# Optimization experiments

Measured on AMD Instinct MI355X. Metric: run time of the kernel, lower is better.

## Reference

```python
import jax, jax.numpy as jnp
import numpy as np


def segment_softmax(scores, seg, num_segments):
    # numerically stable softmax over edges grouped by destination node
    m = jax.ops.segment_max(scores, seg, num_segments=num_segments)
    e = jnp.exp(scores - m[seg])
    d = jax.ops.segment_sum(e, seg, num_segments=num_segments)
    return e / d[seg]


def setup_inputs() -> dict:
    key = jax.random.key(0)
    ks = jax.random.split(key, 13)
    N, E, D = 50000, 400000, 128
    s = 0.02
    return {
        "x": jax.random.normal(ks[0], (N, D), dtype=jnp.float32),
        "t": jax.random.normal(ks[1], (N, D), dtype=jnp.float32),
        "edge_index": jax.random.randint(ks[2], (2, E), 0, N),
        "W_x": jax.random.normal(ks[3], (D, D), dtype=jnp.float32) * s,
        "W_t": jax.random.normal(ks[4], (D, D), dtype=jnp.float32) * s,
        "Q_alpha_w": jax.random.normal(ks[5], (D, D), dtype=jnp.float32) * s,
        "Q_alpha_b": jax.random.normal(ks[6], (D,), dtype=jnp.float32) * s,
        "K_alpha_w": jax.random.normal(ks[7], (D, D), dtype=jnp.float32) * s,
        "K_alpha_b": jax.random.normal(ks[8], (D,), dtype=jnp.float32) * s,
        "Q_beta_w": jax.random.normal(ks[9], (D, D), dtype=jnp.float32) * s,
        "Q_beta_b": jax.random.normal(ks[10], (D,), dtype=jnp.float32) * s,
        "K_beta_w": jax.random.normal(ks[11], (D, D), dtype=jnp.float32) * s,
        "K_beta_b": jax.random.normal(ks[12], (D,), dtype=jnp.float32) * s,
    }


def reference(x, t, edge_index, W_x, W_t, Q_alpha_w, Q_alpha_b,
              K_alpha_w, K_alpha_b, Q_beta_w, Q_beta_b, K_beta_w, K_beta_b):
    N, D = x.shape
    row, col = edge_index[0], edge_index[1]  # row = dest (i), col = src (j)
    inv_sqrt_d = 1.0 / (D ** 0.5)

    # Linear projections on nodes, then gather per edge (same math as
    # projecting the gathered edge features, since Linear is per-row).
    q_alpha = (t @ Q_alpha_w.T + Q_alpha_b)[row]   # [E, D]
    k_alpha = (t @ K_alpha_w.T + K_alpha_b)[col]   # [E, D]
    alpha_scores = jnp.sum(q_alpha * k_alpha, axis=-1) * inv_sqrt_d  # [E]
    alpha = segment_softmax(alpha_scores, row, N)  # [E]

    q_beta = (x @ Q_beta_w.T + Q_beta_b)[row]
    k_beta = (x @ K_beta_w.T + K_beta_b)[col]
    beta_scores = jnp.sum(q_beta * k_beta, axis=-1) * inv_sqrt_d
    beta = segment_softmax(beta_scores, row, N)

    msg_for_t = alpha[:, None] * (t @ W_t.T)[col]  # [E, D]
    msg_for_x = beta[:, None] * (x @ W_x.T)[col]   # [E, D]

    out_x = jax.ops.segment_sum(msg_for_x, row, num_segments=N)  # [N, D]
    out_t = jax.ops.segment_sum(msg_for_t, row, num_segments=N)  # [N, D]
    return (out_x, out_t)
```

## Files before the change

kernel.cpp:

```cpp
#include <hip/hip_runtime.h>

__device__ __forceinline__ unsigned short f2bf(float f) {
    unsigned int x = __float_as_uint(f);
    x += 0x7fffu + ((x >> 16) & 1u);
    return (unsigned short)(x >> 16);
}
__device__ __forceinline__ float2 bf2x(unsigned int u) {
    float2 r;
    r.x = __uint_as_float(u << 16);
    r.y = __uint_as_float(u & 0xffff0000u);
    return r;
}
__device__ __forceinline__ float bcastf(float v, int l) {
    return __uint_as_float(__builtin_amdgcn_readlane(__float_as_uint(v), l));
}
template <int PAT>
__device__ __forceinline__ float swzadd(float v) {
    return v + __uint_as_float(__builtin_amdgcn_ds_swizzle(__float_as_uint(v), PAT));
}

typedef __attribute__((ext_vector_type(8))) short frag8;
typedef __attribute__((ext_vector_type(4))) float fragf4;

__global__ __launch_bounds__(256) void convert_hist(
    const float* __restrict__ s0, const float* __restrict__ s1,
    const float* __restrict__ s2, const float* __restrict__ s3,
    const float* __restrict__ s4, const float* __restrict__ s5,
    unsigned short* __restrict__ dst,
    const int* __restrict__ row, int* __restrict__ deg, int E)
{
    const int b = blockIdx.x;
    if (b < 96) {
        int id = b * 256 + threadIdx.x;
        int m = id >> 12;
        int e = (id & 4095) * 4;
        const float* s = (m == 0) ? s0 : (m == 1) ? s1 : (m == 2) ? s2
                       : (m == 3) ? s3 : (m == 4) ? s4 : s5;
        float4 v = *(const float4*)(s + e);
        int r = e >> 7, c = e & 127;
        int ct = r >> 4, li = r & 15;
        int ks = c >> 5, quad = (c >> 3) & 3, j = c & 7;
        ushort4 u;
        u.x = f2bf(v.x); u.y = f2bf(v.y); u.z = f2bf(v.z); u.w = f2bf(v.w);
        *(ushort4*)(dst + m * 16384 +
                    ((size_t)((ct * 4 + ks) * 64 + quad * 16 + li)) * 8 + j) = u;
    } else {
        int e = (b - 96) * 256 + threadIdx.x;
        if (e < E) atomicAdd(&deg[row[e]], 1);
    }
}

#define TLROW 72
__global__ __launch_bounds__(256, 4) void proj_scatter(
    const float* __restrict__ in_t, const float* __restrict__ in_x, int N,
    const unsigned short* __restrict__ Wbf,
    const float* __restrict__ Qa_b, const float* __restrict__ Ka_b,
    const float* __restrict__ Qb_b, const float* __restrict__ Kb_b,
    unsigned short* __restrict__ qa, unsigned short* __restrict__ qb,
    unsigned short* __restrict__ kab, unsigned short* __restrict__ twxw,
    const int* __restrict__ erow, const int* __restrict__ ecol,
    int* __restrict__ cursor, int* __restrict__ csr_col, int E,
    int nScat, int nbx)
{
    __shared__ __align__(16) unsigned short tile[4][2][16 * TLROW];

    if ((int)blockIdx.x < nScat) {
        int e = blockIdx.x * 256 + threadIdx.x;
        if (e < E) {
            int p = atomicAdd(&cursor[erow[e]], 1);
            csr_col[p] = ecol[e];
        }
        return;
    }
    const int pb = blockIdx.x - nScat;
    const int bx = pb % nbx;
    const int rest = pb / nbx;
    const int p = rest & 1;
    const int cth = rest >> 1;

    const int wave = threadIdx.x >> 6;
    const int lane = threadIdx.x & 63;
    const int li = lane & 15, quad = lane >> 4;
    const int r0 = (bx * 4 + wave) * 16;
    if (r0 >= N) return;
    const int r = r0 + li;
    const bool rv = r < N;

    frag8 bt[4];
    {
        const float* inp = p ? in_x : in_t;
        const float* st = inp + (size_t)r * 128 + quad * 8;
#pragma unroll
        for (int ks = 0; ks < 4; ks++) {
            float4 lo = make_float4(0.f, 0.f, 0.f, 0.f), hi = lo;
            if (rv) {
                lo = *(const float4*)(st + ks * 32);
                hi = *(const float4*)(st + ks * 32 + 4);
            }
            frag8 f;
            f[0] = (short)f2bf(lo.x); f[1] = (short)f2bf(lo.y);
            f[2] = (short)f2bf(lo.z); f[3] = (short)f2bf(lo.w);
            f[4] = (short)f2bf(hi.x); f[5] = (short)f2bf(hi.y);
            f[6] = (short)f2bf(hi.z); f[7] = (short)f2bf(hi.w);
            bt[ks] = f;
        }
    }

    int buf = 0;
    auto phase = [&](int m, const float* bias,
                     unsigned short* dst, int rstride, int coff) {
        const unsigned short* wb = Wbf + (size_t)m * 16384 + (size_t)cth * 8192
                                 + (size_t)lane * 8;
        frag8 af[16];
#pragma unroll
        for (int u = 0; u < 16; u++)
            af[u] = *(const frag8*)(wb + u * 512);

        fragf4 acc[4];
#pragma unroll
        for (int ct = 0; ct < 4; ct++) acc[ct] = (fragf4){0.f, 0.f, 0.f, 0.f};
#pragma unroll
        for (int ct = 0; ct < 4; ct++) {
#pragma unroll
            for (int ks = 0; ks < 4; ks++)
                acc[ct] = __builtin_amdgcn_mfma_f32_16x16x32_bf16(
                    af[ct * 4 + ks], bt[ks], acc[ct], 0, 0, 0);
        }

        unsigned short* lt = &tile[wave][buf][0];
#pragma unroll
        for (int ct = 0; ct < 4; ct++) {
            const int c = ct * 16 + quad * 4;
            float4 bv = make_float4(0.f, 0.f, 0.f, 0.f);
            if (bias) bv = *(const float4*)(bias + cth * 64 + c);
            ushort4 u;
            u.x = f2bf(acc[ct][0] + bv.x);
            u.y = f2bf(acc[ct][1] + bv.y);
            u.z = f2bf(acc[ct][2] + bv.z);
            u.w = f2bf(acc[ct][3] + bv.w);
            *(ushort4*)&lt[li * TLROW + c] = u;
        }
#pragma unroll
        for (int it = 0; it < 2; it++) {
            const int rr = it * 8 + (lane >> 3);
            const int cg = lane & 7;
            if (r0 + rr < N) {
                uint4 v = *(const uint4*)&lt[rr * TLROW + cg * 8];
                *(uint4*)(dst + (size_t)(r0 + rr) * rstride + coff + cg * 8) = v;
            }
        }
        buf ^= 1;
    };

    const int ch = cth * 64;
    if (p == 0) {
        phase(0, Qa_b, qa,   128, ch);
        phase(1, Ka_b, kab,  256, ch);
        phase(2, nullptr, twxw, 256, ch);
    } else {
        phase(3, Qb_b, qb,   128, ch);
        phase(4, Kb_b, kab,  256, 128 + ch);
        phase(5, nullptr, twxw, 256, 128 + ch);
    }
}

#define SCAN_CHUNK 2048

__device__ __forceinline__ int wave_incl_scan(int v, int lane) {
#pragma unroll
    for (int d = 1; d < 64; d <<= 1) {
        int u = __shfl_up(v, d, 64);
        if (lane >= d) v += u;
    }
    return v;
}

__global__ __launch_bounds__(256) void scan_partial(const int* __restrict__ deg,
                                                    int* __restrict__ partial, int N) {
    const int tid = threadIdx.x;
    const int base = blockIdx.x * SCAN_CHUNK + tid * 8;
    int s = 0;
#pragma unroll
    for (int j = 0; j < 8; j++) {
        int i = base + j;
        s += (i < N) ? deg[i] : 0;
    }
    const int lane = tid & 63;
    s = wave_incl_scan(s, lane);
    __shared__ int wsum[4];
    if (lane == 63) wsum[tid >> 6] = s;
    __syncthreads();
    if (tid == 0) partial[blockIdx.x] = wsum[0] + wsum[1] + wsum[2] + wsum[3];
}

__global__ __launch_bounds__(64) void scan_base(int* __restrict__ partial, int nb,
                                                int* __restrict__ offs, int N) {
    const int lane = threadIdx.x;
    int v = (lane < nb) ? partial[lane] : 0;
    int inc = wave_incl_scan(v, lane);
    if (lane < nb) partial[lane] = inc - v;
    if (lane == 63) offs[N] = inc;
}

__global__ __launch_bounds__(256) void scan_final(const int* __restrict__ deg,
                                                  const int* __restrict__ partial,
                                                  int* __restrict__ offs,
                                                  int* __restrict__ cursor, int N) {
    const int tid = threadIdx.x;
    const int lane = tid & 63;
    const int wv = tid >> 6;
    const int base = blockIdx.x * SCAN_CHUNK + tid * 8;
    int v[8];
    int s = 0;
#pragma unroll
    for (int j = 0; j < 8; j++) {
        int i = base + j;
        v[j] = (i < N) ? deg[i] : 0;
        s += v[j];
    }
    int incl = wave_incl_scan(s, lane);
    __shared__ int wsum[4];
    if (lane == 63) wsum[wv] = incl;
    __syncthreads();
    int wbase = 0;
#pragma unroll
    for (int w = 0; w < 4; w++) wbase += (w < wv) ? wsum[w] : 0;
    int run = partial[blockIdx.x] + wbase + incl - s;
#pragma unroll
    for (int j = 0; j < 8; j++) {
        int i = base + j;
        if (i < N) { offs[i] = run; cursor[i] = run; }
        run += v[j];
    }
}

__global__ __launch_bounds__(256) void edge_fused(
    const unsigned short* __restrict__ qa, const unsigned short* __restrict__ qb,
    const unsigned short* __restrict__ kab, const unsigned short* __restrict__ twxw,
    const int* __restrict__ csr_col, const int* __restrict__ offs,
    float* __restrict__ out_x, float* __restrict__ out_t, int N)
{
    const int n = blockIdx.x * 4 + (threadIdx.x >> 6);
    if (n >= N) return;
    const int lane = threadIdx.x & 63;
    const int g = lane >> 4, sub = lane & 15;
    const int s = offs[n], end = offs[n + 1];

    float qaf[8], qbf[8];
    {
        uint4 a = *(const uint4*)(qa + (size_t)n * 128 + sub * 8);
        uint4 b = *(const uint4*)(qb + (size_t)n * 128 + sub * 8);
        float2 f;
        f = bf2x(a.x); qaf[0] = f.x; qaf[1] = f.y;
        f = bf2x(a.y); qaf[2] = f.x; qaf[3] = f.y;
        f = bf2x(a.z); qaf[4] = f.x; qaf[5] = f.y;
        f = bf2x(a.w); qaf[6] = f.x; qaf[7] = f.y;
        f = bf2x(b.x); qbf[0] = f.x; qbf[1] = f.y;
        f = bf2x(b.y); qbf[2] = f.x; qbf[3] = f.y;
        f = bf2x(b.z); qbf[4] = f.x; qbf[5] = f.y;
        f = bf2x(b.w); qbf[6] = f.x; qbf[7] = f.y;
    }

    const float scale = 0.08838834764831845f;
    const bool xside = lane >= 32;
    const unsigned short* vbase = twxw + lane * 4;
    float acc0 = 0.f, acc1 = 0.f, acc2 = 0.f, acc3 = 0.f, dd = 0.f;

    if (end > s) {
        int c = csr_col[min(s + g, end - 1)];
        for (int i0 = s; i0 < end; i0 += 4) {
            const bool val = (i0 + g) < end;
            const int idx = i0 + 4 + g;
            const int cn = csr_col[(idx < end) ? idx : (end - 1)];

            const int c0 = __builtin_amdgcn_readlane(c, 0);
            const int c1 = __builtin_amdgcn_readlane(c, 16);
            const int c2 = __builtin_amdgcn_readlane(c, 32);
            const int c3 = __builtin_amdgcn_readlane(c, 48);
            const uint2 gv0 = *(const uint2*)(vbase + (size_t)c0 * 256);
            const uint2 gv1 = *(const uint2*)(vbase + (size_t)c1 * 256);
            const uint2 gv2 = *(const uint2*)(vbase + (size_t)c2 * 256);
            const uint2 gv3 = *(const uint2*)(vbase + (size_t)c3 * 256);

            const unsigned short* kp = kab + (size_t)c * 256 + sub * 8;
            const uint4 ka4 = *(const uint4*)kp;
            const uint4 kb4 = *(const uint4*)(kp + 128);
            float pa = 0.f, pb = 0.f;
            {
                float2 f;
                f = bf2x(ka4.x); pa = fmaf(qaf[0], f.x, fmaf(qaf[1], f.y, pa));
                f = bf2x(ka4.y); pa = fmaf(qaf[2], f.x, fmaf(qaf[3], f.y, pa));
                f = bf2x(ka4.z); pa = fmaf(qaf[4], f.x, fmaf(qaf[5], f.y, pa));
                f = bf2x(ka4.w); pa = fmaf(qaf[6], f.x, fmaf(qaf[7], f.y, pa));
                f = bf2x(kb4.x); pb = fmaf(qbf[0], f.x, fmaf(qbf[1], f.y, pb));
                f = bf2x(kb4.y); pb = fmaf(qbf[2], f.x, fmaf(qbf[3], f.y, pb));
                f = bf2x(kb4.z); pb = fmaf(qbf[4], f.x, fmaf(qbf[5], f.y, pb));
                f = bf2x(kb4.w); pb = fmaf(qbf[6], f.x, fmaf(qbf[7], f.y, pb));
            }
            pa = swzadd<0x041F>(pa); pb = swzadd<0x041F>(pb);
            pa = swzadd<0x081F>(pa); pb = swzadd<0x081F>(pb);
            pa = swzadd<0x101F>(pa); pb = swzadd<0x101F>(pb);
            pa = swzadd<0x201F>(pa); pb = swzadd<0x201F>(pb);

            const float ea = val ? __expf(fminf(pa * scale, 60.f)) : 0.f;
            const float eb = val ? __expf(fminf(pb * scale, 60.f)) : 0.f;

            const float w0 = xside ? bcastf(eb, 0)  : bcastf(ea, 0);
            const float w1 = xside ? bcastf(eb, 16) : bcastf(ea, 16);
            const float w2 = xside ? bcastf(eb, 32) : bcastf(ea, 32);
            const float w3 = xside ? bcastf(eb, 48) : bcastf(ea, 48);

            float2 lo, hi;
            lo = bf2x(gv0.x); hi = bf2x(gv0.y);
            dd += w0;
            acc0 = fmaf(w0, lo.x, acc0); acc1 = fmaf(w0, lo.y, acc1);
            acc2 = fmaf(w0, hi.x, acc2); acc3 = fmaf(w0, hi.y, acc3);
            lo = bf2x(gv1.x); hi = bf2x(gv1.y);
            dd += w1;
            acc0 = fmaf(w1, lo.x, acc0); acc1 = fmaf(w1, lo.y, acc1);
            acc2 = fmaf(w1, hi.x, acc2); acc3 = fmaf(w1, hi.y, acc3);
            lo = bf2x(gv2.x); hi = bf2x(gv2.y);
            dd += w2;
            acc0 = fmaf(w2, lo.x, acc0); acc1 = fmaf(w2, lo.y, acc1);
            acc2 = fmaf(w2, hi.x, acc2); acc3 = fmaf(w2, hi.y, acc3);
            lo = bf2x(gv3.x); hi = bf2x(gv3.y);
            dd += w3;
            acc0 = fmaf(w3, lo.x, acc0); acc1 = fmaf(w3, lo.y, acc1);
            acc2 = fmaf(w3, hi.x, acc2); acc3 = fmaf(w3, hi.y, acc3);

            c = cn;
        }
    }

    const float r = (dd > 0.f) ? 1.f / dd : 0.f;
    float4 o = make_float4(acc0 * r, acc1 * r, acc2 * r, acc3 * r);
    float* op = xside ? (out_x + (size_t)n * 128 + (lane - 32) * 4)
                      : (out_t + (size_t)n * 128 + lane * 4);
    *(float4*)op = o;
}

extern "C" void kernel_launch(void* const* d_in, const int* in_sizes, int n_in,
                              void* d_out, int out_size, void* d_ws, size_t ws_size,
                              hipStream_t stream) {
    const float* x    = (const float*)d_in[0];
    const float* t    = (const float*)d_in[1];
    const int*   ei   = (const int*)d_in[2];
    const float* W_x  = (const float*)d_in[3];
    const float* W_t  = (const float*)d_in[4];
    const float* Qa_w = (const float*)d_in[5];
    const float* Qa_b = (const float*)d_in[6];
    const float* Ka_w = (const float*)d_in[7];
    const float* Ka_b = (const float*)d_in[8];
    const float* Qb_w = (const float*)d_in[9];
    const float* Qb_b = (const float*)d_in[10];
    const float* Kb_w = (const float*)d_in[11];
    const float* Kb_b = (const float*)d_in[12];

    const int N = in_sizes[0] / 128;
    const int E = in_sizes[2] / 2;
    const int* row = ei;
    const int* col = ei + E;

    char* ws = (char*)d_ws;
    size_t off = 0;
    auto carve = [&](size_t bytes) -> void* {
        void* p = ws + off;
        off += (bytes + 255) & ~(size_t)255;
        return p;
    };
    unsigned short* qa   = (unsigned short*)carve((size_t)N * 128 * 2);
    unsigned short* qb   = (unsigned short*)carve((size_t)N * 128 * 2);
    unsigned short* kab  = (unsigned short*)carve((size_t)N * 256 * 2);
    unsigned short* twxw = (unsigned short*)carve((size_t)N * 256 * 2);
    int* deg      = (int*)carve((size_t)N * 4);
    int* cursor   = (int*)carve((size_t)N * 4);
    int* offs     = (int*)carve((size_t)(N + 1) * 4);
    int* csr_col  = (int*)carve((size_t)E * 4);
    const int nscan = (N + SCAN_CHUNK - 1) / SCAN_CHUNK;
    int* partial  = (int*)carve((size_t)nscan * 4);
    unsigned short* Wbf = (unsigned short*)carve((size_t)6 * 16384 * 2);

    (void)hipMemsetAsync(deg, 0, (size_t)N * 4, stream);

    dim3 b256(256);
    const int nHist = (E + 255) / 256;
    convert_hist<<<dim3(96 + nHist), b256, 0, stream>>>(
        Qa_w, Ka_w, W_t, Qb_w, Kb_w, W_x, Wbf, row, deg, E);

    scan_partial<<<dim3(nscan), b256, 0, stream>>>(deg, partial, N);
    scan_base<<<dim3(1), dim3(64), 0, stream>>>(partial, nscan, offs, N);
    scan_final<<<dim3(nscan), b256, 0, stream>>>(deg, partial, offs, cursor, N);

    const int nbx = (N + 63) / 64;
    const int nScat = (E + 255) / 256;
    proj_scatter<<<dim3(nScat + nbx * 4), b256, 0, stream>>>(
        t, x, N, Wbf, Qa_b, Ka_b, Qb_b, Kb_b, qa, qb, kab, twxw,
        row, col, cursor, csr_col, E, nScat, nbx);

    float* out_x = (float*)d_out;
    float* out_t = out_x + (size_t)N * 128;
    edge_fused<<<dim3((N + 3) / 4), b256, 0, stream>>>(
        qa, qb, kab, twxw, csr_col, offs, out_x, out_t, N);
}
```

Baseline: 262.7 us.

## Fold key projection into query weights and apply value projection after aggregation

Precomputes Wq^T·Wk (scaled) and Wk^T·bq so the score becomes (q')·t_j on raw bf16 node features, removing the per-node key projections. The key bias is dropped because it is constant within each softmax segment. The edge kernel now gathers only raw t/x rows (512 B per edge instead of separate key and value gathers) and aggregates with one node per 16-lane group. The W_t/W_x projection is then applied per 16-node tile with MFMA after aggregation, by linearity. This cuts projection work and gather traffic, at the cost of extra bf16 rounding of raw features and aggregates, and less parallelism per node in the edge loop.

```diff
diff --git a/kernel.cpp b/kernel.cpp
--- a/kernel.cpp
+++ b/kernel.cpp
@@ -11,9 +11,6 @@
     r.y = __uint_as_float(u & 0xffff0000u);
     return r;
 }
-__device__ __forceinline__ float bcastf(float v, int l) {
-    return __uint_as_float(__builtin_amdgcn_readlane(__float_as_uint(v), l));
-}
 template <int PAT>
 __device__ __forceinline__ float swzadd(float v) {
     return v + __uint_as_float(__builtin_amdgcn_ds_swizzle(__float_as_uint(v), PAT));
@@ -22,30 +19,86 @@
 typedef __attribute__((ext_vector_type(8))) short frag8;
 typedef __attribute__((ext_vector_type(4))) float fragf4;
 
-__global__ __launch_bounds__(256) void convert_hist(
-    const float* __restrict__ s0, const float* __restrict__ s1,
-    const float* __restrict__ s2, const float* __restrict__ s3,
-    const float* __restrict__ s4, const float* __restrict__ s5,
-    unsigned short* __restrict__ dst,
+
+__global__ __launch_bounds__(256) void prep_convert_hist(
+    const float* __restrict__ Qa_w, const float* __restrict__ Ka_w,
+    const float* __restrict__ Qa_b,
+    const float* __restrict__ Qb_w, const float* __restrict__ Kb_w,
+    const float* __restrict__ Qb_b,
+    const float* __restrict__ W_t, const float* __restrict__ W_x,
+    unsigned short* __restrict__ Wbf, float* __restrict__ ba, float* __restrict__ bb,
     const int* __restrict__ row, int* __restrict__ deg, int E)
 {
     const int b = blockIdx.x;
-    if (b < 96) {
-        int id = b * 256 + threadIdx.x;
-        int m = id >> 12;
-        int e = (id & 4095) * 4;
-        const float* s = (m == 0) ? s0 : (m == 1) ? s1 : (m == 2) ? s2
-                       : (m == 3) ? s3 : (m == 4) ? s4 : s5;
-        float4 v = *(const float4*)(s + e);
-        int r = e >> 7, c = e & 127;
+    const int tid = threadIdx.x;
+    const float sc = 0.08838834764831845f;
+
+    if (b < 2) {
+        const int m = b;
+        const float* Kw = m ? Kb_w : Ka_w;
+        const float* Qw = m ? Qb_w : Qa_w;
+        const float* bq = m ? Qb_b : Qa_b;
+        const int r0l = (tid & 31) * 4;
+        const int c0l = (tid >> 5) * 16;
+        float a0[16], a1[16], a2[16], a3[16];
+#pragma unroll
+        for (int j = 0; j < 16; j++) { a0[j] = 0.f; a1[j] = 0.f; a2[j] = 0.f; a3[j] = 0.f; }
+#pragma unroll 2
+        for (int ch = 0; ch < 128; ch++) {
+            const float* kr = Kw + ch * 128;
+            const float* qr = Qw + ch * 128;
+            float4 kv = *(const float4*)(kr + r0l);
+            float4 q0 = *(const float4*)(qr + c0l);
+            float4 q1 = *(const float4*)(qr + c0l + 4);
+            float4 q2v = *(const float4*)(qr + c0l + 8);
+            float4 q3 = *(const float4*)(qr + c0l + 12);
+            float qv[16] = {q0.x,q0.y,q0.z,q0.w, q1.x,q1.y,q1.z,q1.w,
+                            q2v.x,q2v.y,q2v.z,q2v.w, q3.x,q3.y,q3.z,q3.w};
+#pragma unroll
+            for (int j = 0; j < 16; j++) {
+                a0[j] = fmaf(kv.x, qv[j], a0[j]);
+                a1[j] = fmaf(kv.y, qv[j], a1[j]);
+                a2[j] = fmaf(kv.z, qv[j], a2[j]);
+                a3[j] = fmaf(kv.w, qv[j], a3[j]);
+            }
+        }
+        unsigned short* base = Wbf + (size_t)m * 16384;
+#pragma unroll
+        for (int i = 0; i < 4; i++) {
+            const float* ai = (i == 0) ? a0 : (i == 1) ? a1 : (i == 2) ? a2 : a3;
+            const int r = r0l + i, ct = r >> 4, li = r & 15;
+#pragma unroll
+            for (int jb = 0; jb < 2; jb++) {
+                const int c = c0l + jb * 8;
+                const int ks = c >> 5, quad = (c >> 3) & 3;
+                frag8 u;
+#pragma unroll
+                for (int j = 0; j < 8; j++) u[j] = (short)f2bf(ai[jb * 8 + j] * sc);
+                *(frag8*)(base + ((size_t)((ct * 4 + ks) * 64 + quad * 16 + li)) * 8) = u;
+            }
+        }
+        if (tid < 128) {
+            float a = 0.f;
+#pragma unroll 8
+            for (int ch = 0; ch < 128; ch++) a = fmaf(bq[ch], Kw[ch * 128 + tid], a);
+            (m ? bb : ba)[tid] = a * sc;
+        }
+    } else if (b < 34) {
+        const int cm = (b - 2) >> 4;
+        const int local = (b - 2) & 15;
+        const int id = local * 256 + tid;
+        const int e4 = id * 4;
+        const float* s = cm ? W_x : W_t;
+        float4 v = *(const float4*)(s + e4);
+        int r = e4 >> 7, c = e4 & 127;
         int ct = r >> 4, li = r & 15;
         int ks = c >> 5, quad = (c >> 3) & 3, j = c & 7;
         ushort4 u;
         u.x = f2bf(v.x); u.y = f2bf(v.y); u.z = f2bf(v.z); u.w = f2bf(v.w);
-        *(ushort4*)(dst + m * 16384 +
+        *(ushort4*)(Wbf + (size_t)(2 + cm) * 16384 +
                     ((size_t)((ct * 4 + ks) * 64 + quad * 16 + li)) * 8 + j) = u;
     } else {
-        int e = (b - 96) * 256 + threadIdx.x;
+        int e = (b - 34) * 256 + tid;
         if (e < E) atomicAdd(&deg[row[e]], 1);
     }
 }
@@ -54,15 +107,13 @@
 __global__ __launch_bounds__(256, 4) void proj_scatter(
     const float* __restrict__ in_t, const float* __restrict__ in_x, int N,
     const unsigned short* __restrict__ Wbf,
-    const float* __restrict__ Qa_b, const float* __restrict__ Ka_b,
-    const float* __restrict__ Qb_b, const float* __restrict__ Kb_b,
-    unsigned short* __restrict__ qa, unsigned short* __restrict__ qb,
-    unsigned short* __restrict__ kab, unsigned short* __restrict__ twxw,
+    const float* __restrict__ ba, const float* __restrict__ bb,
+    unsigned short* __restrict__ q2ab, unsigned short* __restrict__ txb,
     const int* __restrict__ erow, const int* __restrict__ ecol,
     int* __restrict__ cursor, int* __restrict__ csr_col, int E,
     int nScat, int nbx)
 {
-    __shared__ __align__(16) unsigned short tile[4][2][16 * TLROW];
+    __shared__ __align__(16) unsigned short tile[4][16 * TLROW];
 
     if ((int)blockIdx.x < nScat) {
         int e = blockIdx.x * 256 + threadIdx.x;
@@ -106,61 +157,52 @@
         }
     }
 
-    int buf = 0;
-    auto phase = [&](int m, const float* bias,
-                     unsigned short* dst, int rstride, int coff) {
-        const unsigned short* wb = Wbf + (size_t)m * 16384 + (size_t)cth * 8192
-                                 + (size_t)lane * 8;
-        frag8 af[16];
-#pragma unroll
-        for (int u = 0; u < 16; u++)
-            af[u] = *(const frag8*)(wb + u * 512);
-
-        fragf4 acc[4];
-#pragma unroll
-        for (int ct = 0; ct < 4; ct++) acc[ct] = (fragf4){0.f, 0.f, 0.f, 0.f};
-#pragma unroll
-        for (int ct = 0; ct < 4; ct++) {
-#pragma unroll
-            for (int ks = 0; ks < 4; ks++)
-                acc[ct] = __builtin_amdgcn_mfma_f32_16x16x32_bf16(
-                    af[ct * 4 + ks], bt[ks], acc[ct], 0, 0, 0);
-        }
-
-        unsigned short* lt = &tile[wave][buf][0];
-#pragma unroll
-        for (int ct = 0; ct < 4; ct++) {
-            const int c = ct * 16 + quad * 4;
-            float4 bv = make_float4(0.f, 0.f, 0.f, 0.f);
-            if (bias) bv = *(const float4*)(bias + cth * 64 + c);
-            ushort4 u;
-            u.x = f2bf(acc[ct][0] + bv.x);
-            u.y = f2bf(acc[ct][1] + bv.y);
-            u.z = f2bf(acc[ct][2] + bv.z);
-            u.w = f2bf(acc[ct][3] + bv.w);
-            *(ushort4*)&lt[li * TLROW + c] = u;
-        }
-#pragma unroll
-        for (int it = 0; it < 2; it++) {
-            const int rr = it * 8 + (lane >> 3);
-            const int cg = lane & 7;
-            if (r0 + rr < N) {
-                uint4 v = *(const uint4*)&lt[rr * TLROW + cg * 8];
-                *(uint4*)(dst + (size_t)(r0 + rr) * rstride + coff + cg * 8) = v;
-            }
-        }
-        buf ^= 1;
-    };
-
-    const int ch = cth * 64;
-    if (p == 0) {
-        phase(0, Qa_b, qa,   128, ch);
-        phase(1, Ka_b, kab,  256, ch);
-        phase(2, nullptr, twxw, 256, ch);
-    } else {
-        phase(3, Qb_b, qb,   128, ch);
-        phase(4, Kb_b, kab,  256, 128 + ch);
-        phase(5, nullptr, twxw, 256, 128 + ch);
+    if (cth == 0 && rv) {
+#pragma unroll
+        for (int ks = 0; ks < 4; ks++)
+            *(frag8*)(txb + (size_t)r * 256 + p * 128 + ks * 32 + quad * 8) = bt[ks];
+    }
+
+    const unsigned short* wb = Wbf + (size_t)p * 16384 + (size_t)cth * 8192
+                             + (size_t)lane * 8;
+    frag8 af[16];
+#pragma unroll
+    for (int u = 0; u < 16; u++)
+        af[u] = *(const frag8*)(wb + u * 512);
+
+    fragf4 acc[4];
+#pragma unroll
+    for (int ct = 0; ct < 4; ct++) acc[ct] = (fragf4){0.f, 0.f, 0.f, 0.f};
+#pragma unroll
+    for (int ct = 0; ct < 4; ct++) {
+#pragma unroll
+        for (int ks = 0; ks < 4; ks++)
+            acc[ct] = __builtin_amdgcn_mfma_f32_16x16x32_bf16(
+                af[ct * 4 + ks], bt[ks], acc[ct], 0, 0, 0);
+    }
+
+    const float* bias = (p ? bb : ba) + cth * 64;
+    unsigned short* lt = &tile[wave][0];
+#pragma unroll
+    for (int ct = 0; ct < 4; ct++) {
+        const int c = ct * 16 + quad * 4;
+        float4 bv = *(const float4*)(bias + c);
+        ushort4 u;
+        u.x = f2bf(acc[ct][0] + bv.x);
+        u.y = f2bf(acc[ct][1] + bv.y);
+        u.z = f2bf(acc[ct][2] + bv.z);
+        u.w = f2bf(acc[ct][3] + bv.w);
+        *(ushort4*)&lt[li * TLROW + c] = u;
+    }
+    const int coff = p * 128 + cth * 64;
+#pragma unroll
+    for (int it = 0; it < 2; it++) {
+        const int rr = it * 8 + (lane >> 3);
+        const int cg = lane & 7;
+        if (r0 + rr < N) {
+            uint4 v = *(const uint4*)&lt[rr * TLROW + cg * 8];
+            *(uint4*)(q2ab + (size_t)(r0 + rr) * 256 + coff + cg * 8) = v;
+        }
     }
 }
 
@@ -235,108 +277,134 @@
 }
 
 __global__ __launch_bounds__(256) void edge_fused(
-    const unsigned short* __restrict__ qa, const unsigned short* __restrict__ qb,
-    const unsigned short* __restrict__ kab, const unsigned short* __restrict__ twxw,
+    const unsigned short* __restrict__ q2ab, const unsigned short* __restrict__ txb,
+    const unsigned short* __restrict__ Wbf,
     const int* __restrict__ csr_col, const int* __restrict__ offs,
     float* __restrict__ out_x, float* __restrict__ out_t, int N)
 {
-    const int n = blockIdx.x * 4 + (threadIdx.x >> 6);
-    if (n >= N) return;
-    const int lane = threadIdx.x & 63;
+    __shared__ __align__(16) unsigned short tile[16][264];
+    const int tid = threadIdx.x;
+    const int wv = tid >> 6, lane = tid & 63;
     const int g = lane >> 4, sub = lane & 15;
-    const int s = offs[n], end = offs[n + 1];
-
-    float qaf[8], qbf[8];
-    {
-        uint4 a = *(const uint4*)(qa + (size_t)n * 128 + sub * 8);
-        uint4 b = *(const uint4*)(qb + (size_t)n * 128 + sub * 8);
+    const int nblk = blockIdx.x * 16;
+    if (nblk >= N) return;
+    const int n = nblk + wv * 4 + g;
+    const bool nv = n < N;
+
+    float qa_r[8], qb_r[8];
+    if (nv) {
+        uint4 a = *(const uint4*)(q2ab + (size_t)n * 256 + sub * 8);
+        uint4 b = *(const uint4*)(q2ab + (size_t)n * 256 + 128 + sub * 8);
         float2 f;
-        f = bf2x(a.x); qaf[0] = f.x; qaf[1] = f.y;
-        f = bf2x(a.y); qaf[2] = f.x; qaf[3] = f.y;
-        f = bf2x(a.z); qaf[4] = f.x; qaf[5] = f.y;
-        f = bf2x(a.w); qaf[6] = f.x; qaf[7] = f.y;
-        f = bf2x(b.x); qbf[0] = f.x; qbf[1] = f.y;
-        f = bf2x(b.y); qbf[2] = f.x; qbf[3] = f.y;
-        f = bf2x(b.z); qbf[4] = f.x; qbf[5] = f.y;
-        f = bf2x(b.w); qbf[6] = f.x; qbf[7] = f.y;
-    }
-
-    const float scale = 0.08838834764831845f;
-    const bool xside = lane >= 32;
-    const unsigned short* vbase = twxw + lane * 4;
-    float acc0 = 0.f, acc1 = 0.f, acc2 = 0.f, acc3 = 0.f, dd = 0.f;
-
-    if (end > s) {
-        int c = csr_col[min(s + g, end - 1)];
-        for (int i0 = s; i0 < end; i0 += 4) {
-            const bool val = (i0 + g) < end;
-            const int idx = i0 + 4 + g;
-            const int cn = csr_col[(idx < end) ? idx : (end - 1)];
-
-            const int c0 = __builtin_amdgcn_readlane(c, 0);
-            const int c1 = __builtin_amdgcn_readlane(c, 16);
-            const int c2 = __builtin_amdgcn_readlane(c, 32);
-            const int c3 = __builtin_amdgcn_readlane(c, 48);
-            const uint2 gv0 = *(const uint2*)(vbase + (size_t)c0 * 256);
-            const uint2 gv1 = *(const uint2*)(vbase + (size_t)c1 * 256);
-            const uint2 gv2 = *(const uint2*)(vbase + (size_t)c2 * 256);
-            const uint2 gv3 = *(const uint2*)(vbase + (size_t)c3 * 256);
-
-            const unsigned short* kp = kab + (size_t)c * 256 + sub * 8;
-            const uint4 ka4 = *(const uint4*)kp;
-            const uint4 kb4 = *(const uint4*)(kp + 128);
+        f = bf2x(a.x); qa_r[0] = f.x; qa_r[1] = f.y;
+        f = bf2x(a.y); qa_r[2] = f.x; qa_r[3] = f.y;
+        f = bf2x(a.z); qa_r[4] = f.x; qa_r[5] = f.y;
+        f = bf2x(a.w); qa_r[6] = f.x; qa_r[7] = f.y;
+        f = bf2x(b.x); qb_r[0] = f.x; qb_r[1] = f.y;
+        f = bf2x(b.y); qb_r[2] = f.x; qb_r[3] = f.y;
+        f = bf2x(b.z); qb_r[4] = f.x; qb_r[5] = f.y;
+        f = bf2x(b.w); qb_r[6] = f.x; qb_r[7] = f.y;
+    } else {
+#pragma unroll
+        for (int j = 0; j < 8; j++) { qa_r[j] = 0.f; qb_r[j] = 0.f; }
+    }
+
+    int s = 0, e = 0;
+    if (nv) { s = offs[n]; e = offs[n + 1]; }
+
+    float aggt[8], aggx[8];
+#pragma unroll
+    for (int j = 0; j < 8; j++) { aggt[j] = 0.f; aggx[j] = 0.f; }
+    float dda = 0.f, ddb = 0.f;
+
+    if (e > s) {
+        int c = csr_col[s];
+        const unsigned short* rp = txb + (size_t)c * 256;
+        uint4 t8 = *(const uint4*)(rp + sub * 8);
+        uint4 x8 = *(const uint4*)(rp + 128 + sub * 8);
+        for (int i = s; i < e; i++) {
+            const int inx = (i + 1 < e) ? i + 1 : i;
+            const int cn = csr_col[inx];
+            const unsigned short* rn = txb + (size_t)cn * 256;
+            uint4 t8n = *(const uint4*)(rn + sub * 8);
+            uint4 x8n = *(const uint4*)(rn + 128 + sub * 8);
+
+            float tv[8], xv[8];
+            float2 f;
+            f = bf2x(t8.x); tv[0] = f.x; tv[1] = f.y;
+            f = bf2x(t8.y); tv[2] = f.x; tv[3] = f.y;
+            f = bf2x(t8.z); tv[4] = f.x; tv[5] = f.y;
+            f = bf2x(t8.w); tv[6] = f.x; tv[7] = f.y;
+            f = bf2x(x8.x); xv[0] = f.x; xv[1] = f.y;
+            f = bf2x(x8.y); xv[2] = f.x; xv[3] = f.y;
+            f = bf2x(x8.z); xv[4] = f.x; xv[5] = f.y;
+            f = bf2x(x8.w); xv[6] = f.x; xv[7] = f.y;
+
             float pa = 0.f, pb = 0.f;
-            {
-                float2 f;
-                f = bf2x(ka4.x); pa = fmaf(qaf[0], f.x, fmaf(qaf[1], f.y, pa));
-                f = bf2x(ka4.y); pa = fmaf(qaf[2], f.x, fmaf(qaf[3], f.y, pa));
-                f = bf2x(ka4.z); pa = fmaf(qaf[4], f.x, fmaf(qaf[5], f.y, pa));
-                f = bf2x(ka4.w); pa = fmaf(qaf[6], f.x, fmaf(qaf[7], f.y, pa));
-                f = bf2x(kb4.x); pb = fmaf(qbf[0], f.x, fmaf(qbf[1], f.y, pb));
-                f = bf2x(kb4.y); pb = fmaf(qbf[2], f.x, fmaf(qbf[3], f.y, pb));
-                f = bf2x(kb4.z); pb = fmaf(qbf[4], f.x, fmaf(qbf[5], f.y, pb));
-                f = bf2x(kb4.w); pb = fmaf(qbf[6], f.x, fmaf(qbf[7], f.y, pb));
+#pragma unroll
+            for (int j = 0; j < 8; j++) {
+                pa = fmaf(qa_r[j], tv[j], pa);
+                pb = fmaf(qb_r[j], xv[j], pb);
             }
             pa = swzadd<0x041F>(pa); pb = swzadd<0x041F>(pb);
             pa = swzadd<0x081F>(pa); pb = swzadd<0x081F>(pb);
             pa = swzadd<0x101F>(pa); pb = swzadd<0x101F>(pb);
             pa = swzadd<0x201F>(pa); pb = swzadd<0x201F>(pb);
 
-            const float ea = val ? __expf(fminf(pa * scale, 60.f)) : 0.f;
-            const float eb = val ? __expf(fminf(pb * scale, 60.f)) : 0.f;
-
-            const float w0 = xside ? bcastf(eb, 0)  : bcastf(ea, 0);
-            const float w1 = xside ? bcastf(eb, 16) : bcastf(ea, 16);
-            const float w2 = xside ? bcastf(eb, 32) : bcastf(ea, 32);
-            const float w3 = xside ? bcastf(eb, 48) : bcastf(ea, 48);
-
-            float2 lo, hi;
-            lo = bf2x(gv0.x); hi = bf2x(gv0.y);
-            dd += w0;
-            acc0 = fmaf(w0, lo.x, acc0); acc1 = fmaf(w0, lo.y, acc1);
-            acc2 = fmaf(w0, hi.x, acc2); acc3 = fmaf(w0, hi.y, acc3);
-            lo = bf2x(gv1.x); hi = bf2x(gv1.y);
-            dd += w1;
-            acc0 = fmaf(w1, lo.x, acc0); acc1 = fmaf(w1, lo.y, acc1);
-            acc2 = fmaf(w1, hi.x, acc2); acc3 = fmaf(w1, hi.y, acc3);
-            lo = bf2x(gv2.x); hi = bf2x(gv2.y);
-            dd += w2;
-            acc0 = fmaf(w2, lo.x, acc0); acc1 = fmaf(w2, lo.y, acc1);
-            acc2 = fmaf(w2, hi.x, acc2); acc3 = fmaf(w2, hi.y, acc3);
-            lo = bf2x(gv3.x); hi = bf2x(gv3.y);
-            dd += w3;
-            acc0 = fmaf(w3, lo.x, acc0); acc1 = fmaf(w3, lo.y, acc1);
-            acc2 = fmaf(w3, hi.x, acc2); acc3 = fmaf(w3, hi.y, acc3);
-
-            c = cn;
-        }
-    }
-
-    const float r = (dd > 0.f) ? 1.f / dd : 0.f;
-    float4 o = make_float4(acc0 * r, acc1 * r, acc2 * r, acc3 * r);
-    float* op = xside ? (out_x + (size_t)n * 128 + (lane - 32) * 4)
-                      : (out_t + (size_t)n * 128 + lane * 4);
-    *(float4*)op = o;
+            const float ea = __expf(fminf(pa, 60.f));
+            const float eb = __expf(fminf(pb, 60.f));
+            dda += ea; ddb += eb;
+#pragma unroll
+            for (int j = 0; j < 8; j++) {
+                aggt[j] = fmaf(ea, tv[j], aggt[j]);
+                aggx[j] = fmaf(eb, xv[j], aggx[j]);
+            }
+            t8 = t8n; x8 = x8n;
+        }
+    }
+
+    const float ra = (dda > 0.f) ? 1.f / dda : 0.f;
+    const float rb = (ddb > 0.f) ? 1.f / ddb : 0.f;
+    const int rowi = wv * 4 + g;
+    frag8 ut, ux;
+#pragma unroll
+    for (int j = 0; j < 8; j++) {
+        ut[j] = (short)f2bf(aggt[j] * ra);
+        ux[j] = (short)f2bf(aggx[j] * rb);
+    }
+    *(frag8*)&tile[rowi][sub * 8] = ut;
+    *(frag8*)&tile[rowi][128 + sub * 8] = ux;
+    __syncthreads();
+
+    const int m = wv >> 1, chunk = wv & 1;
+    const int li = lane & 15, quad = lane >> 4;
+    frag8 bt[4];
+#pragma unroll
+    for (int ks = 0; ks < 4; ks++)
+        bt[ks] = *(const frag8*)&tile[li][m * 128 + ks * 32 + quad * 8];
+    const unsigned short* wbp = Wbf + (size_t)(2 + m) * 16384 + (size_t)chunk * 8192
+                              + (size_t)lane * 8;
+    frag8 af[16];
+#pragma unroll
+    for (int u = 0; u < 16; u++)
+        af[u] = *(const frag8*)(wbp + u * 512);
+    fragf4 acc[4];
+#pragma unroll
+    for (int ct = 0; ct < 4; ct++) acc[ct] = (fragf4){0.f, 0.f, 0.f, 0.f};
+#pragma unroll
+    for (int ct = 0; ct < 4; ct++) {
+#pragma unroll
+        for (int ks = 0; ks < 4; ks++)
+            acc[ct] = __builtin_amdgcn_mfma_f32_16x16x32_bf16(
+                af[ct * 4 + ks], bt[ks], acc[ct], 0, 0, 0);
+    }
+    if (nblk + li < N) {
+        float* outp = (m ? out_x : out_t) + (size_t)(nblk + li) * 128 + chunk * 64;
+#pragma unroll
+        for (int ct = 0; ct < 4; ct++)
+            *(float4*)(outp + ct * 16 + quad * 4) =
+                make_float4(acc[ct][0], acc[ct][1], acc[ct][2], acc[ct][3]);
+    }
 }
 
 extern "C" void kernel_launch(void* const* d_in, const int* in_sizes, int n_in,
@@ -350,11 +418,9 @@
     const float* Qa_w = (const float*)d_in[5];
     const float* Qa_b = (const float*)d_in[6];
     const float* Ka_w = (const float*)d_in[7];
-    const float* Ka_b = (const float*)d_in[8];
     const float* Qb_w = (const float*)d_in[9];
     const float* Qb_b = (const float*)d_in[10];
     const float* Kb_w = (const float*)d_in[11];
-    const float* Kb_b = (const float*)d_in[12];
 
     const int N = in_sizes[0] / 128;
     const int E = in_sizes[2] / 2;
@@ -368,24 +434,24 @@
         off += (bytes + 255) & ~(size_t)255;
         return p;
     };
-    unsigned short* qa   = (unsigned short*)carve((size_t)N * 128 * 2);
-    unsigned short* qb   = (unsigned short*)carve((size_t)N * 128 * 2);
-    unsigned short* kab  = (unsigned short*)carve((size_t)N * 256 * 2);
-    unsigned short* twxw = (unsigned short*)carve((size_t)N * 256 * 2);
+    unsigned short* q2ab = (unsigned short*)carve((size_t)N * 256 * 2);
+    unsigned short* txb  = (unsigned short*)carve((size_t)N * 256 * 2);
     int* deg      = (int*)carve((size_t)N * 4);
     int* cursor   = (int*)carve((size_t)N * 4);
     int* offs     = (int*)carve((size_t)(N + 1) * 4);
     int* csr_col  = (int*)carve((size_t)E * 4);
     const int nscan = (N + SCAN_CHUNK - 1) / SCAN_CHUNK;
     int* partial  = (int*)carve((size_t)nscan * 4);
-    unsigned short* Wbf = (unsigned short*)carve((size_t)6 * 16384 * 2);
+    unsigned short* Wbf = (unsigned short*)carve((size_t)4 * 16384 * 2);
+    float* ba = (float*)carve(128 * 4);
+    float* bb = (float*)carve(128 * 4);
 
     (void)hipMemsetAsync(deg, 0, (size_t)N * 4, stream);
 
     dim3 b256(256);
     const int nHist = (E + 255) / 256;
-    convert_hist<<<dim3(96 + nHist), b256, 0, stream>>>(
-        Qa_w, Ka_w, W_t, Qb_w, Kb_w, W_x, Wbf, row, deg, E);
+    prep_convert_hist<<<dim3(34 + nHist), b256, 0, stream>>>(
+        Qa_w, Ka_w, Qa_b, Qb_w, Kb_w, Qb_b, W_t, W_x, Wbf, ba, bb, row, deg, E);
 
     scan_partial<<<dim3(nscan), b256, 0, stream>>>(deg, partial, N);
     scan_base<<<dim3(1), dim3(64), 0, stream>>>(partial, nscan, offs, N);
@@ -394,11 +460,11 @@
     const int nbx = (N + 63) / 64;
     const int nScat = (E + 255) / 256;
     proj_scatter<<<dim3(nScat + nbx * 4), b256, 0, stream>>>(
-        t, x, N, Wbf, Qa_b, Ka_b, Qb_b, Kb_b, qa, qb, kab, twxw,
+        t, x, N, Wbf, ba, bb, q2ab, txb,
         row, col, cursor, csr_col, E, nScat, nbx);
 
     float* out_x = (float*)d_out;
     float* out_t = out_x + (size_t)N * 128;
-    edge_fused<<<dim3((N + 3) / 4), b256, 0, stream>>>(
-        qa, qb, kab, twxw, csr_col, offs, out_x, out_t, N);
-}
+    edge_fused<<<dim3((N + 15) / 16), b256, 0, stream>>>(
+        q2ab, txb, Wbf, csr_col, offs, out_x, out_t, N);
+}
```

Result: slower. 294.6 us (+12.1%).
